# Kernel optimization log

Measured on AMD Instinct MI355X. Metric: run time of the kernel, lower is better.

Reference implementation:

```python
import jax, jax.numpy as jnp
import numpy as np

B, L, C = 8, 8192, 512

def setup_inputs() -> dict:
    key = jax.random.key(0)
    kq, kk, kv_, kw = jax.random.split(key, 4)
    q = jax.random.normal(kq, (B, L, C), dtype=jnp.float32)
    k = jax.random.normal(kk, (B, L, C), dtype=jnp.float32)
    v = jax.random.normal(kv_, (B, L, C), dtype=jnp.float32)
    W = jax.random.normal(kw, (C, C), dtype=jnp.float32) * (1.0 / np.sqrt(C))
    b = jnp.zeros((C,), dtype=jnp.float32)
    return {"q": q, "k": k, "v": v, "W": W, "b": b}

def reference(q, k, v, W, b):
    # L2-normalize q and k over channel dim (matches torch x / x.norm(dim=-1, keepdim=True))
    qn = q / jnp.linalg.norm(q, axis=-1, keepdims=True)
    kn = k / jnp.linalg.norm(k, axis=-1, keepdims=True)
    # kv = k * v, dropout is identity (p=0 / eval); global sum over sequence
    kv_sum = jnp.sum(kn * v, axis=-2, keepdims=True)  # [B, 1, C]
    out = kv_sum * qn                                  # [B, L, C]
    # output Linear: out @ W^T + b (torch nn.Linear convention, W:[out,in])
    return jnp.einsum('blc,oc->blo', out, W) + b
```

## Files before the change

kernel.cpp:

```cpp
#include <hip/hip_runtime.h>
#include <hip/hip_bf16.h>
#include <stdint.h>

#define B_ 8
#define L_ 8192
#define C_ 512

typedef short bf16x8 __attribute__((ext_vector_type(8)));
typedef float f32x4 __attribute__((ext_vector_type(4)));

#define GAS(p) ((const __attribute__((address_space(1))) void*)(p))
#define LAS(p) ((__attribute__((address_space(3))) void*)(p))

__global__ __launch_bounds__(256)
void kv_reduce(const float* __restrict__ kin, const float* __restrict__ vin,
               float* __restrict__ kv) {
    const int bi   = blockIdx.x;
    const int b    = bi >> 8;
    const int row0 = (bi & 255) * 32;
    const int lane = threadIdx.x & 63;
    const int wave = threadIdx.x >> 6;

    const f32x4* kb = (const f32x4*)(kin + ((size_t)b * L_ + row0) * C_);
    const f32x4* vb = (const f32x4*)(vin + ((size_t)b * L_ + row0) * C_);

    f32x4 acca = {0.f,0.f,0.f,0.f}, accb = {0.f,0.f,0.f,0.f};

    #pragma unroll 1
    for (int it = 0; it < 2; ++it) {
        const int r0 = wave * 8 + it * 4;
        f32x4 ka[4], kc[4], va[4], vc[4];
        #pragma unroll
        for (int j = 0; j < 4; ++j) {
            const f32x4* krow = kb + (size_t)(r0 + j) * (C_/4);
            ka[j] = __builtin_nontemporal_load(krow + lane);
            kc[j] = __builtin_nontemporal_load(krow + 64 + lane);
        }
        #pragma unroll
        for (int j = 0; j < 4; ++j) {
            const f32x4* vrow = vb + (size_t)(r0 + j) * (C_/4);
            va[j] = __builtin_nontemporal_load(vrow + lane);
            vc[j] = __builtin_nontemporal_load(vrow + 64 + lane);
        }
        float ss[4];
        #pragma unroll
        for (int j = 0; j < 4; ++j)
            ss[j] = ka[j][0]*ka[j][0] + ka[j][1]*ka[j][1] + ka[j][2]*ka[j][2] + ka[j][3]*ka[j][3]
                  + kc[j][0]*kc[j][0] + kc[j][1]*kc[j][1] + kc[j][2]*kc[j][2] + kc[j][3]*kc[j][3];
        #pragma unroll
        for (int m = 32; m >= 1; m >>= 1) {
            #pragma unroll
            for (int j = 0; j < 4; ++j) ss[j] += __shfl_xor(ss[j], m);
        }
        #pragma unroll
        for (int j = 0; j < 4; ++j) {
            const float inv = rsqrtf(ss[j]);
            #pragma unroll
            for (int x = 0; x < 4; ++x) {
                acca[x] += ka[j][x] * inv * va[j][x];
                accb[x] += kc[j][x] * inv * vc[j][x];
            }
        }
    }

    __shared__ __align__(16) float red[4][C_];
    ((f32x4*)&red[wave][0])[lane]      = acca;
    ((f32x4*)&red[wave][0])[64 + lane] = accb;
    __syncthreads();
    for (int c = threadIdx.x; c < C_; c += 256) {
        float s = red[0][c] + red[1][c] + red[2][c] + red[3][c];
        atomicAdd(&kv[b * C_ + c], s);
    }
}

__global__ __launch_bounds__(256)
void prep_w(const float* __restrict__ W, const float* __restrict__ kv,
            __hip_bfloat16* __restrict__ Wb) {
    int idx = blockIdx.x * 256 + threadIdx.x;
    int e   = idx << 2;
    int b   = e >> 18;
    int oc  = e & 0x3FFFF;
    int c   = oc & (C_ - 1);
    float4 w4 = *(const float4*)(W + oc);
    float4 s4 = *(const float4*)(kv + b * C_ + c);
    union { __hip_bfloat16 h[4]; uint2 u; } pk;
    pk.h[0] = __float2bfloat16(w4.x * s4.x);
    pk.h[1] = __float2bfloat16(w4.y * s4.y);
    pk.h[2] = __float2bfloat16(w4.z * s4.z);
    pk.h[3] = __float2bfloat16(w4.w * s4.w);
    *(uint2*)(Wb + e) = pk.u;
}

__global__ __launch_bounds__(256, 2)
void gemm_out(const float* __restrict__ qin, const __hip_bfloat16* __restrict__ Wb,
              const float* __restrict__ bias, float* __restrict__ out) {
    const int blk   = blockIdx.x;
    const int xcd   = blk & 7;
    const int local = blk >> 3;
    const int n0    = (local & 3) * 128;
    const int m0    = (xcd * 64 + (local >> 2)) * 128;
    const int b     = m0 >> 13;
    const int tid  = threadIdx.x;
    const int lane = tid & 63;
    const int wave = tid >> 6;

    __shared__ __align__(16) unsigned short As[2][128 * 64];
    __shared__ __align__(16) unsigned short Bs[2][128 * 64];
    __shared__ float s_inv[128];

    const int aj  = tid & 7;
    const int arp = tid >> 3;
    const float* qbase = qin + (size_t)m0 * C_;
    const __hip_bfloat16* WbB = Wb + ((size_t)b * C_ + n0) * C_;

    const int r16 = lane & 15;
    const int qd  = lane >> 4;
    const int wm  = wave & 1;
    const int wn  = wave >> 1;

    f32x4 acc[4][4];
    #pragma unroll
    for (int i = 0; i < 4; ++i)
        #pragma unroll
        for (int j = 0; j < 4; ++j)
            acc[i][j] = (f32x4){0.f, 0.f, 0.f, 0.f};

    float ssq[4] = {0.f, 0.f, 0.f, 0.f};
    float4 xa[4], xb[4];

    auto stageB = [&](int buf, int kc) {
        #pragma unroll
        for (int i = 0; i < 4; ++i) {
            int cid = i * 256 + wave * 64 + lane;
            int n   = cid >> 3;
            int cj  = cid & 7;
            int kk  = ((cj ^ (n & 7)) << 3);
            const __hip_bfloat16* g = WbB + (size_t)n * C_ + kc + kk;
            __builtin_amdgcn_global_load_lds(GAS(g),
                LAS(&Bs[buf][(i * 256 + wave * 64) * 8]), 16, 0, 0);
        }
    };
    auto loadA = [&](int kc) {
        #pragma unroll
        for (int p = 0; p < 4; ++p) {
            const float* g = qbase + (size_t)(p * 32 + arp) * C_ + kc + aj * 8;
            xa[p] = ((const float4*)g)[0];
            xb[p] = ((const float4*)g)[1];
        }
    };
    auto writeA = [&](int buf) {
        #pragma unroll
        for (int p = 0; p < 4; ++p) {
            int m = p * 32 + arp;
            float4 x0 = xa[p], x1 = xb[p];
            ssq[p] += x0.x*x0.x + x0.y*x0.y + x0.z*x0.z + x0.w*x0.w
                    + x1.x*x1.x + x1.y*x1.y + x1.z*x1.z + x1.w*x1.w;
            union { __hip_bfloat16 h[8]; uint4 u; } pk;
            pk.h[0] = __float2bfloat16(x0.x); pk.h[1] = __float2bfloat16(x0.y);
            pk.h[2] = __float2bfloat16(x0.z); pk.h[3] = __float2bfloat16(x0.w);
            pk.h[4] = __float2bfloat16(x1.x); pk.h[5] = __float2bfloat16(x1.y);
            pk.h[6] = __float2bfloat16(x1.z); pk.h[7] = __float2bfloat16(x1.w);
            *(uint4*)&As[buf][m * 64 + ((aj ^ (m & 7)) << 3)] = pk.u;
        }
    };
    auto compute = [&](int buf) {
        #pragma unroll
        for (int ks = 0; ks < 2; ++ks) {
            bf16x8 af[4], bfr[4];
            #pragma unroll
            for (int t = 0; t < 4; ++t) {
                int m = wm * 64 + t * 16 + r16;
                af[t]  = *(const bf16x8*)&As[buf][m * 64 + (((ks * 4 + qd) ^ (m & 7)) << 3)];
                int n = wn * 64 + t * 16 + r16;
                bfr[t] = *(const bf16x8*)&Bs[buf][n * 64 + (((ks * 4 + qd) ^ (n & 7)) << 3)];
            }
            #pragma unroll
            for (int mt = 0; mt < 4; ++mt)
                #pragma unroll
                for (int nt = 0; nt < 4; ++nt)
                    acc[mt][nt] = __builtin_amdgcn_mfma_f32_16x16x32_bf16(
                        af[mt], bfr[nt], acc[mt][nt], 0, 0, 0);
        }
    };

    stageB(0, 0);
    loadA(0);
    writeA(0);
    __syncthreads();

    #pragma unroll
    for (int t = 0; t < 7; ++t) {
        const int cur = t & 1, nxt = cur ^ 1;
        stageB(nxt, (t + 1) * 64);
        loadA((t + 1) * 64);
        compute(cur);
        writeA(nxt);
        __syncthreads();
    }
    compute(1);

    #pragma unroll
    for (int p = 0; p < 4; ++p) {
        float s = ssq[p];
        s += __shfl_xor(s, 1);
        s += __shfl_xor(s, 2);
        s += __shfl_xor(s, 4);
        if (aj == 0) s_inv[p * 32 + arp] = rsqrtf(s);
    }
    __syncthreads();

    #pragma unroll
    for (int nt = 0; nt < 4; ++nt) {
        int col  = n0 + wn * 64 + nt * 16 + r16;
        float bv = bias[col];
        #pragma unroll
        for (int mt = 0; mt < 4; ++mt) {
            int rl = wm * 64 + mt * 16 + qd * 4;
            float4 inv4 = *(const float4*)&s_inv[rl];
            float* op = out + (size_t)(m0 + rl) * C_ + col;
            op[0]      = acc[mt][nt][0] * inv4.x + bv;
            op[C_]     = acc[mt][nt][1] * inv4.y + bv;
            op[2 * C_] = acc[mt][nt][2] * inv4.z + bv;
            op[3 * C_] = acc[mt][nt][3] * inv4.w + bv;
        }
    }
}

extern "C" void kernel_launch(void* const* d_in, const int* in_sizes, int n_in,
                              void* d_out, int out_size, void* d_ws, size_t ws_size,
                              hipStream_t stream) {
    const float* q    = (const float*)d_in[0];
    const float* k    = (const float*)d_in[1];
    const float* v    = (const float*)d_in[2];
    const float* W    = (const float*)d_in[3];
    const float* bias = (const float*)d_in[4];
    float* out = (float*)d_out;

    float* kv = (float*)d_ws;
    __hip_bfloat16* Wb = (__hip_bfloat16*)((char*)d_ws + 16384);

    hipMemsetAsync(kv, 0, B_ * C_ * sizeof(float), stream);
    kv_reduce<<<2048, 256, 0, stream>>>(k, v, kv);
    prep_w<<<2048, 256, 0, stream>>>(W, kv, Wb);
    gemm_out<<<2048, 256, 0, stream>>>(q, Wb, bias, out);
}
```

Measured before the change: 473.4 us.

## Prenormalize q to bf16 in reduction kernel and stage GEMM A via direct LDS loads

After: 412.9 us. 12.8% less time.

```diff
diff --git a/kernel.cpp b/kernel.cpp
--- a/kernel.cpp
+++ b/kernel.cpp
@@ -13,8 +13,9 @@
 #define LAS(p) ((__attribute__((address_space(3))) void*)(p))
 
 __global__ __launch_bounds__(256)
-void kv_reduce(const float* __restrict__ kin, const float* __restrict__ vin,
-               float* __restrict__ kv) {
+void kv_qnorm(const float* __restrict__ kin, const float* __restrict__ vin,
+              const float* __restrict__ qin, float* __restrict__ kv,
+              __hip_bfloat16* __restrict__ qb) {
     const int bi   = blockIdx.x;
     const int b    = bi >> 8;
     const int row0 = (bi & 255) * 32;
@@ -60,6 +61,46 @@
                 acca[x] += ka[j][x] * inv * va[j][x];
                 accb[x] += kc[j][x] * inv * vc[j][x];
             }
+        }
+    }
+
+    const f32x4* qg = (const f32x4*)(qin + ((size_t)b * L_ + row0) * C_);
+    __hip_bfloat16* qbo = qb + ((size_t)b * L_ + row0) * C_;
+    #pragma unroll 1
+    for (int it = 0; it < 2; ++it) {
+        const int r0 = wave * 8 + it * 4;
+        f32x4 qa[4], qc[4];
+        #pragma unroll
+        for (int j = 0; j < 4; ++j) {
+            const f32x4* qrow = qg + (size_t)(r0 + j) * (C_/4);
+            qa[j] = __builtin_nontemporal_load(qrow + lane);
+            qc[j] = __builtin_nontemporal_load(qrow + 64 + lane);
+        }
+        float ss[4];
+        #pragma unroll
+        for (int j = 0; j < 4; ++j)
+            ss[j] = qa[j][0]*qa[j][0] + qa[j][1]*qa[j][1] + qa[j][2]*qa[j][2] + qa[j][3]*qa[j][3]
+                  + qc[j][0]*qc[j][0] + qc[j][1]*qc[j][1] + qc[j][2]*qc[j][2] + qc[j][3]*qc[j][3];
+        #pragma unroll
+        for (int m = 32; m >= 1; m >>= 1) {
+            #pragma unroll
+            for (int j = 0; j < 4; ++j) ss[j] += __shfl_xor(ss[j], m);
+        }
+        #pragma unroll
+        for (int j = 0; j < 4; ++j) {
+            const float inv = rsqrtf(ss[j]);
+            union { __hip_bfloat16 h[4]; uint2 u; } p0, p1;
+            p0.h[0] = __float2bfloat16(qa[j][0] * inv);
+            p0.h[1] = __float2bfloat16(qa[j][1] * inv);
+            p0.h[2] = __float2bfloat16(qa[j][2] * inv);
+            p0.h[3] = __float2bfloat16(qa[j][3] * inv);
+            p1.h[0] = __float2bfloat16(qc[j][0] * inv);
+            p1.h[1] = __float2bfloat16(qc[j][1] * inv);
+            p1.h[2] = __float2bfloat16(qc[j][2] * inv);
+            p1.h[3] = __float2bfloat16(qc[j][3] * inv);
+            uint2* dst = (uint2*)(qbo + (size_t)(r0 + j) * C_);
+            dst[lane]      = p0.u;
+            dst[64 + lane] = p1.u;
         }
     }
 
@@ -92,7 +133,7 @@
 }
 
 __global__ __launch_bounds__(256, 2)
-void gemm_out(const float* __restrict__ qin, const __hip_bfloat16* __restrict__ Wb,
+void gemm_out(const __hip_bfloat16* __restrict__ qbin, const __hip_bfloat16* __restrict__ Wb,
               const float* __restrict__ bias, float* __restrict__ out) {
     const int blk   = blockIdx.x;
     const int xcd   = blk & 7;
@@ -106,12 +147,9 @@
 
     __shared__ __align__(16) unsigned short As[2][128 * 64];
     __shared__ __align__(16) unsigned short Bs[2][128 * 64];
-    __shared__ float s_inv[128];
-
-    const int aj  = tid & 7;
-    const int arp = tid >> 3;
-    const float* qbase = qin + (size_t)m0 * C_;
-    const __hip_bfloat16* WbB = Wb + ((size_t)b * C_ + n0) * C_;
+
+    const __hip_bfloat16* Abase = qbin + (size_t)m0 * C_;
+    const __hip_bfloat16* Bbase = Wb + ((size_t)b * C_ + n0) * C_;
 
     const int r16 = lane & 15;
     const int qd  = lane >> 4;
@@ -125,42 +163,17 @@
         for (int j = 0; j < 4; ++j)
             acc[i][j] = (f32x4){0.f, 0.f, 0.f, 0.f};
 
-    float ssq[4] = {0.f, 0.f, 0.f, 0.f};
-    float4 xa[4], xb[4];
-
-    auto stageB = [&](int buf, int kc) {
+    auto stage = [&](int buf, int kc) {
         #pragma unroll
         for (int i = 0; i < 4; ++i) {
             int cid = i * 256 + wave * 64 + lane;
-            int n   = cid >> 3;
+            int r   = cid >> 3;
             int cj  = cid & 7;
-            int kk  = ((cj ^ (n & 7)) << 3);
-            const __hip_bfloat16* g = WbB + (size_t)n * C_ + kc + kk;
-            __builtin_amdgcn_global_load_lds(GAS(g),
+            int kk  = ((cj ^ (r & 7)) << 3);
+            __builtin_amdgcn_global_load_lds(GAS(Abase + (size_t)r * C_ + kc + kk),
+                LAS(&As[buf][(i * 256 + wave * 64) * 8]), 16, 0, 0);
+            __builtin_amdgcn_global_load_lds(GAS(Bbase + (size_t)r * C_ + kc + kk),
                 LAS(&Bs[buf][(i * 256 + wave * 64) * 8]), 16, 0, 0);
-        }
-    };
-    auto loadA = [&](int kc) {
-        #pragma unroll
-        for (int p = 0; p < 4; ++p) {
-            const float* g = qbase + (size_t)(p * 32 + arp) * C_ + kc + aj * 8;
-            xa[p] = ((const float4*)g)[0];
-            xb[p] = ((const float4*)g)[1];
-        }
-    };
-    auto writeA = [&](int buf) {
-        #pragma unroll
-        for (int p = 0; p < 4; ++p) {
-            int m = p * 32 + arp;
-            float4 x0 = xa[p], x1 = xb[p];
-            ssq[p] += x0.x*x0.x + x0.y*x0.y + x0.z*x0.z + x0.w*x0.w
-                    + x1.x*x1.x + x1.y*x1.y + x1.z*x1.z + x1.w*x1.w;
-            union { __hip_bfloat16 h[8]; uint4 u; } pk;
-            pk.h[0] = __float2bfloat16(x0.x); pk.h[1] = __float2bfloat16(x0.y);
-            pk.h[2] = __float2bfloat16(x0.z); pk.h[3] = __float2bfloat16(x0.w);
-            pk.h[4] = __float2bfloat16(x1.x); pk.h[5] = __float2bfloat16(x1.y);
-            pk.h[6] = __float2bfloat16(x1.z); pk.h[7] = __float2bfloat16(x1.w);
-            *(uint4*)&As[buf][m * 64 + ((aj ^ (m & 7)) << 3)] = pk.u;
         }
     };
     auto compute = [&](int buf) {
@@ -183,31 +196,15 @@
         }
     };
 
-    stageB(0, 0);
-    loadA(0);
-    writeA(0);
+    stage(0, 0);
     __syncthreads();
-
     #pragma unroll
     for (int t = 0; t < 7; ++t) {
-        const int cur = t & 1, nxt = cur ^ 1;
-        stageB(nxt, (t + 1) * 64);
-        loadA((t + 1) * 64);
-        compute(cur);
-        writeA(nxt);
+        stage((t & 1) ^ 1, (t + 1) * 64);
+        compute(t & 1);
         __syncthreads();
     }
     compute(1);
-
-    #pragma unroll
-    for (int p = 0; p < 4; ++p) {
-        float s = ssq[p];
-        s += __shfl_xor(s, 1);
-        s += __shfl_xor(s, 2);
-        s += __shfl_xor(s, 4);
-        if (aj == 0) s_inv[p * 32 + arp] = rsqrtf(s);
-    }
-    __syncthreads();
 
     #pragma unroll
     for (int nt = 0; nt < 4; ++nt) {
@@ -216,12 +213,11 @@
         #pragma unroll
         for (int mt = 0; mt < 4; ++mt) {
             int rl = wm * 64 + mt * 16 + qd * 4;
-            float4 inv4 = *(const float4*)&s_inv[rl];
             float* op = out + (size_t)(m0 + rl) * C_ + col;
-            op[0]      = acc[mt][nt][0] * inv4.x + bv;
-            op[C_]     = acc[mt][nt][1] * inv4.y + bv;
-            op[2 * C_] = acc[mt][nt][2] * inv4.z + bv;
-            op[3 * C_] = acc[mt][nt][3] * inv4.w + bv;
+            op[0]      = acc[mt][nt][0] + bv;
+            op[C_]     = acc[mt][nt][1] + bv;
+            op[2 * C_] = acc[mt][nt][2] + bv;
+            op[3 * C_] = acc[mt][nt][3] + bv;
         }
     }
 }
@@ -238,9 +234,10 @@
 
     float* kv = (float*)d_ws;
     __hip_bfloat16* Wb = (__hip_bfloat16*)((char*)d_ws + 16384);
+    __hip_bfloat16* qb = (__hip_bfloat16*)((char*)d_ws + 16384 + (size_t)B_ * C_ * C_ * 2);
 
     hipMemsetAsync(kv, 0, B_ * C_ * sizeof(float), stream);
-    kv_reduce<<<2048, 256, 0, stream>>>(k, v, kv);
+    kv_qnorm<<<2048, 256, 0, stream>>>(k, v, q, kv, qb);
     prep_w<<<2048, 256, 0, stream>>>(W, kv, Wb);
-    gemm_out<<<2048, 256, 0, stream>>>(q, Wb, bias, out);
-}
+    gemm_out<<<2048, 256, 0, stream>>>(qb, Wb, bias, out);
+}
```
